# Optimization experiments

Hardware: AMD Instinct MI355X
Metric: run time of the kernel (lower is better)

Reference implementation:

```python
import jax, jax.numpy as jnp
import numpy as np

OUT_FEATURES = 11008
IN_FEATURES = 4096
PACKED_LEN = OUT_FEATURES * IN_FEATURES // 4  # 4 ternary vals per byte, 2 bits each


def setup_inputs() -> dict:
    key = jax.random.key(0)
    k1, k2, k3 = jax.random.split(key, 3)
    x = jax.random.normal(k1, (4, 1024, IN_FEATURES), dtype=jnp.float32)
    packed_weight = jax.random.randint(k2, (PACKED_LEN,), 0, 256, dtype=jnp.int32)
    weight_scale = jax.random.uniform(k3, (1,), dtype=jnp.float32)
    return {"x": x, "packed_weight": packed_weight, "weight_scale": weight_scale}


def _dequantize_weight(packed_weight, weight_scale):
    shifts = jnp.arange(0, 8, 2, dtype=jnp.int32)          # [4]
    q = ((packed_weight[:, None] >> shifts) & 3) - 1        # [P, 4]
    q = q.reshape(OUT_FEATURES, IN_FEATURES).astype(jnp.float32)
    return q * weight_scale.reshape(())                      # dequantize


def reference(x, packed_weight, weight_scale):
    w = _dequantize_weight(packed_weight, weight_scale)      # [out, in]
    # F.linear: y = x @ w.T  (bias=False)
    return jnp.einsum('bsi,oi->bso', x, w)
```

## Files before the change

kernel.cpp:

```cpp
#include <hip/hip_runtime.h>
#include <hip/hip_bf16.h>

#define OUT_F 11008
#define IN_F  4096
#define M_DIM 4096

typedef __attribute__((ext_vector_type(8))) short bf16x8;
typedef __attribute__((ext_vector_type(4))) float f32x4;
typedef __attribute__((ext_vector_type(8))) unsigned short us8;

__device__ __forceinline__ unsigned short f2bf_rne(float f) {
    unsigned u = __builtin_bit_cast(unsigned, f);
    u += 0x7fffu + ((u >> 16) & 1u);
    return (unsigned short)(u >> 16);
}

__global__ void prep_kernel(const float* __restrict__ x,
                            unsigned short* __restrict__ xb,
                            const int* __restrict__ pw,
                            unsigned char* __restrict__ pw2) {
    if (blockIdx.x < 8192) {
        size_t i = ((size_t)blockIdx.x * blockDim.x + threadIdx.x) * 8;
        float4 a = *(const float4*)(x + i);
        float4 b = *(const float4*)(x + i + 4);
        us8 o;
        o[0] = f2bf_rne(a.x); o[1] = f2bf_rne(a.y);
        o[2] = f2bf_rne(a.z); o[3] = f2bf_rne(a.w);
        o[4] = f2bf_rne(b.x); o[5] = f2bf_rne(b.y);
        o[6] = f2bf_rne(b.z); o[7] = f2bf_rne(b.w);
        *(us8*)(xb + i) = o;
    } else {
        const int kb   = blockIdx.x - 8192;
        const int kt   = kb & 63;
        const int rgrp = kb >> 6;
        const int row  = rgrp * 256 + threadIdx.x;
        const int4* src = (const int4*)(pw + (size_t)row * 1024 + kt * 16);
        unsigned out[4];
#pragma unroll
        for (int i = 0; i < 4; ++i) {
            int4 v = src[i];
            out[i] = (v.x & 0xFF) | ((v.y & 0xFF) << 8) |
                     ((v.z & 0xFF) << 16) | ((unsigned)v.w << 24);
        }
        *(uint4*)(pw2 + ((size_t)kt * OUT_F + row) * 16) =
            *(const uint4*)out;
    }
}

__device__ __forceinline__ void unpack_byte(unsigned b, unsigned& d_lo,
                                            unsigned& d_hi) {
    const unsigned PA = 0x00800080u;
    const unsigned PB = 0x403F00BFu;
    unsigned m0 = (b & 0xFu) * 0x00404101u;
    unsigned s0 = (m0 & 0x03030303u) | 0x00040004u;
    d_lo = __builtin_amdgcn_perm(PA, PB, s0);
    unsigned m1 = (b >> 4) * 0x00404101u;
    unsigned s1 = (m1 & 0x03030303u) | 0x00040004u;
    d_hi = __builtin_amdgcn_perm(PA, PB, s1);
}

__global__ __launch_bounds__(512, 2) void gemm_kernel(
    const unsigned short* __restrict__ A,
    const unsigned char* __restrict__ P,
    float* __restrict__ C,
    const float* __restrict__ scale_ptr) {
    constexpr int K  = IN_F;
    constexpr int N  = OUT_F;
    constexpr int NT = K / 64;

    __shared__ unsigned short sA[2][2][256][32];
    __shared__ unsigned short sB[2][2][256][32];
    __shared__ unsigned char  pb[2][4096];

    const int tid  = threadIdx.x;
    const int wave = tid >> 6;
    const int lane = tid & 63;
    const int quad = lane >> 4;
    const int mrow = lane & 15;
    const int sw   = quad ^ ((mrow >> 1) & 3);

    const int srow = lane >> 2;
    const int sseg = (lane & 3) ^ ((lane >> 3) & 3);

    const int lin = blockIdx.x;
    const int xcd = lin & 7;
    const int q   = lin >> 3;
    const int bm  = xcd * 2 + q / 43;
    const int bn  = q % 43;

    const int wm = (wave >> 2) * 128;
    const int wn = (wave & 3) * 64;

    const unsigned short* Ag = A + (size_t)bm * 256 * K;

    f32x4 acc[8][4];
#pragma unroll
    for (int i = 0; i < 8; i++)
#pragma unroll
        for (int j = 0; j < 4; j++) acc[i][j] = (f32x4){0.f, 0.f, 0.f, 0.f};

    auto STAGE_A = [&](int nb, int kbase) {
#pragma unroll
        for (int h = 0; h < 2; ++h) {
#pragma unroll
            for (int c = 0; c < 2; ++c) {
                const int chunk = wave * 2 + c;
                const int grow  = chunk * 16 + srow;
                const unsigned short* src =
                    Ag + (size_t)grow * K + kbase + h * 32 + sseg * 8;
                __builtin_amdgcn_global_load_lds(
                    (const __attribute__((address_space(1))) void*)src,
                    (__attribute__((address_space(3))) void*)
                        (&sA[nb][h][0][0] + chunk * 512),
                    16, 0, 0);
            }
        }
    };
    auto STAGE_P = [&](int nb, int kt) {
        if (wave < 4) {
            const unsigned char* src =
                P + ((size_t)kt * N + bn * 256 + wave * 64 + lane) * 16;
            __builtin_amdgcn_global_load_lds(
                (const __attribute__((address_space(1))) void*)src,
                (__attribute__((address_space(3))) void*)(&pb[nb][wave * 1024]),
                16, 0, 0);
        }
    };
    auto UNPACK = [&](int srcb, int dstb) {
        const int row = tid >> 1;
        const int h   = tid & 1;
        unsigned long long pk =
            *(const unsigned long long*)&pb[srcb][tid * 8];
        const int rsw = (row >> 1) & 3;
#pragma unroll
        for (int s = 0; s < 4; ++s) {
            unsigned p16 = (unsigned)(pk >> (16 * s)) & 0xFFFFu;
            unsigned d0, d1, d2, d3;
            unpack_byte(p16 & 0xFFu, d0, d1);
            unpack_byte(p16 >> 8, d2, d3);
            const int slot = s ^ rsw;
            *(uint4*)&sB[dstb][h][row][slot * 8] = (uint4){d0, d1, d2, d3};
        }
    };

    STAGE_A(0, 0);
    STAGE_P(1, 0);
    __syncthreads();
    UNPACK(1, 0);
    STAGE_P(0, 1);
    __syncthreads();

    for (int kt = 0; kt < NT; ++kt) {
        const int  buf  = kt & 1;
        const int  nbuf = buf ^ 1;
        const bool pf1  = (kt + 1 < NT);
        const bool pf2  = (kt + 2 < NT);

        if (pf1) STAGE_A(nbuf, (kt + 1) * 64);
        if (pf2) STAGE_P(nbuf, kt + 2);

        if (pf1) UNPACK(buf, nbuf);

#pragma unroll
        for (int h = 0; h < 2; ++h) {
            bf16x8 a[8], b[4];
#pragma unroll
            for (int t = 0; t < 8; ++t)
                a[t] = *(const bf16x8*)&sA[buf][h][wm + t * 16 + mrow][sw * 8];
#pragma unroll
            for (int j = 0; j < 4; ++j)
                b[j] = *(const bf16x8*)&sB[buf][h][wn + j * 16 + mrow][sw * 8];
#pragma unroll
            for (int t = 0; t < 8; ++t)
#pragma unroll
                for (int j = 0; j < 4; ++j)
                    acc[t][j] = __builtin_amdgcn_mfma_f32_16x16x32_bf16(
                        a[t], b[j], acc[t][j], 0, 0, 0);
        }

        __syncthreads();
    }

    const float scale = *scale_ptr;
    float* Cg = C + (size_t)(bm * 256 + wm) * N + bn * 256 + wn;
#pragma unroll
    for (int i = 0; i < 8; ++i) {
#pragma unroll
        for (int j = 0; j < 4; ++j) {
#pragma unroll
            for (int r = 0; r < 4; ++r) {
                const int row = i * 16 + quad * 4 + r;
                const int col = j * 16 + mrow;
                Cg[(size_t)row * N + col] = acc[i][j][r] * scale;
            }
        }
    }
}

extern "C" void kernel_launch(void* const* d_in, const int* in_sizes, int n_in,
                              void* d_out, int out_size, void* d_ws, size_t ws_size,
                              hipStream_t stream) {
    const float* x   = (const float*)d_in[0];
    const int* pw    = (const int*)d_in[1];
    const float* wsc = (const float*)d_in[2];

    float* out = (float*)d_out;

    unsigned short* xb  = (unsigned short*)d_ws;
    unsigned char*  pw2 = (unsigned char*)((char*)d_ws
                          + (size_t)M_DIM * IN_F * 2);

    prep_kernel<<<8192 + 2752, 256, 0, stream>>>(x, xb, pw, pw2);

    gemm_kernel<<<688, 512, 0, stream>>>(xb, pw2, out, wsc);
}
```

Measured before the change: 620.1 us.

## Pre-swizzle packed weights into MFMA fragment layout and unpack directly into registers

The prep kernel now transposes the packed ternary weights through shared memory into a per-lane MFMA fragment order, so each lane holds a 16-bit pack per (j,h). The GEMM no longer stages packed bytes into LDS, unpacks them into an sB tile, and reads them back. Each wave instead loads its own packed shorts from global memory into registers one tile ahead and unpacks them straight into B fragments. This removes the sB/pb LDS traffic and frees LDS. In exchange each wave of a block repeats unpack work that was shared before, and the global loads are scattered 2-byte accesses.

Result: faster. 558.2 us (-10.0%).

```diff
diff --git a/kernel.cpp b/kernel.cpp
--- a/kernel.cpp
+++ b/kernel.cpp
@@ -18,7 +18,7 @@
 __global__ void prep_kernel(const float* __restrict__ x,
                             unsigned short* __restrict__ xb,
                             const int* __restrict__ pw,
-                            unsigned char* __restrict__ pw2) {
+                            unsigned short* __restrict__ pw2) {
     if (blockIdx.x < 8192) {
         size_t i = ((size_t)blockIdx.x * blockDim.x + threadIdx.x) * 8;
         float4 a = *(const float4*)(x + i);
@@ -30,20 +30,31 @@
         o[6] = f2bf_rne(b.z); o[7] = f2bf_rne(b.w);
         *(us8*)(xb + i) = o;
     } else {
-        const int kb   = blockIdx.x - 8192;
-        const int kt   = kb & 63;
-        const int rgrp = kb >> 6;
-        const int row  = rgrp * 256 + threadIdx.x;
-        const int4* src = (const int4*)(pw + (size_t)row * 1024 + kt * 16);
-        unsigned out[4];
-#pragma unroll
-        for (int i = 0; i < 4; ++i) {
-            int4 v = src[i];
-            out[i] = (v.x & 0xFF) | ((v.y & 0xFF) << 8) |
-                     ((v.z & 0xFF) << 16) | ((unsigned)v.w << 24);
-        }
-        *(uint4*)(pw2 + ((size_t)kt * OUT_F + row) * 16) =
-            *(const uint4*)out;
+        __shared__ unsigned char lb[16 * 1028];
+        const int rg = blockIdx.x - 8192;
+        const int t  = threadIdx.x;
+        const int4* src = (const int4*)(pw + (size_t)rg * 16384);
+#pragma unroll
+        for (int r = 0; r < 16; ++r) {
+            int4 v = src[r * 256 + t];
+            lb[r * 1028 + t * 4 + 0] = (unsigned char)(v.x & 0xFF);
+            lb[r * 1028 + t * 4 + 1] = (unsigned char)(v.y & 0xFF);
+            lb[r * 1028 + t * 4 + 2] = (unsigned char)(v.z & 0xFF);
+            lb[r * 1028 + t * 4 + 3] = (unsigned char)(v.w & 0xFF);
+        }
+        __syncthreads();
+        unsigned short* dst = pw2 + (size_t)rg * 8192;
+#pragma unroll
+        for (int i = 0; i < 32; ++i) {
+            const int u    = i * 256 + t;
+            const int kt   = u >> 7;
+            const int h    = (u >> 6) & 1;
+            const int qd   = (u >> 4) & 3;
+            const int mrow = u & 15;
+            const int c0   = kt * 16 + h * 8 + qd * 2;
+            dst[u] = (unsigned short)(lb[mrow * 1028 + c0] |
+                                      (lb[mrow * 1028 + c0 + 1] << 8));
+        }
     }
 }
 
@@ -59,9 +70,17 @@
     d_hi = __builtin_amdgcn_perm(PA, PB, s1);
 }
 
+__device__ __forceinline__ bf16x8 unpack_us(unsigned short p) {
+    unsigned d0, d1, d2, d3;
+    unpack_byte(p & 0xFFu, d0, d1);
+    unpack_byte((unsigned)p >> 8, d2, d3);
+    uint4 u = (uint4){d0, d1, d2, d3};
+    return __builtin_bit_cast(bf16x8, u);
+}
+
 __global__ __launch_bounds__(512, 2) void gemm_kernel(
     const unsigned short* __restrict__ A,
-    const unsigned char* __restrict__ P,
+    const unsigned short* __restrict__ P,
     float* __restrict__ C,
     const float* __restrict__ scale_ptr) {
     constexpr int K  = IN_F;
@@ -69,8 +88,6 @@
     constexpr int NT = K / 64;
 
     __shared__ unsigned short sA[2][2][256][32];
-    __shared__ unsigned short sB[2][2][256][32];
-    __shared__ unsigned char  pb[2][4096];
 
     const int tid  = threadIdx.x;
     const int wave = tid >> 6;
@@ -92,6 +109,7 @@
     const int wn = (wave & 3) * 64;
 
     const unsigned short* Ag = A + (size_t)bm * 256 * K;
+    const int rgb = bn * 16 + (wn >> 4);
 
     f32x4 acc[8][4];
 #pragma unroll
@@ -116,60 +134,43 @@
             }
         }
     };
-    auto STAGE_P = [&](int nb, int kt) {
-        if (wave < 4) {
-            const unsigned char* src =
-                P + ((size_t)kt * N + bn * 256 + wave * 64 + lane) * 16;
-            __builtin_amdgcn_global_load_lds(
-                (const __attribute__((address_space(1))) void*)src,
-                (__attribute__((address_space(3))) void*)(&pb[nb][wave * 1024]),
-                16, 0, 0);
-        }
+
+    auto pidx = [&](int kt, int j, int h) -> size_t {
+        return (((size_t)(rgb + j) * 64 + kt) * 2 + h) * 64 + lane;
     };
-    auto UNPACK = [&](int srcb, int dstb) {
-        const int row = tid >> 1;
-        const int h   = tid & 1;
-        unsigned long long pk =
-            *(const unsigned long long*)&pb[srcb][tid * 8];
-        const int rsw = (row >> 1) & 3;
-#pragma unroll
-        for (int s = 0; s < 4; ++s) {
-            unsigned p16 = (unsigned)(pk >> (16 * s)) & 0xFFFFu;
-            unsigned d0, d1, d2, d3;
-            unpack_byte(p16 & 0xFFu, d0, d1);
-            unpack_byte(p16 >> 8, d2, d3);
-            const int slot = s ^ rsw;
-            *(uint4*)&sB[dstb][h][row][slot * 8] = (uint4){d0, d1, d2, d3};
-        }
-    };
 
     STAGE_A(0, 0);
-    STAGE_P(1, 0);
-    __syncthreads();
-    UNPACK(1, 0);
-    STAGE_P(0, 1);
+    unsigned short pkb[8], npkb[8];
+#pragma unroll
+    for (int j = 0; j < 4; ++j)
+#pragma unroll
+        for (int h = 0; h < 2; ++h) pkb[j * 2 + h] = P[pidx(0, j, h)];
+#pragma unroll
+    for (int i = 0; i < 8; ++i) npkb[i] = 0;
     __syncthreads();
 
     for (int kt = 0; kt < NT; ++kt) {
         const int  buf  = kt & 1;
         const int  nbuf = buf ^ 1;
         const bool pf1  = (kt + 1 < NT);
-        const bool pf2  = (kt + 2 < NT);
-
-        if (pf1) STAGE_A(nbuf, (kt + 1) * 64);
-        if (pf2) STAGE_P(nbuf, kt + 2);
-
-        if (pf1) UNPACK(buf, nbuf);
+
+        if (pf1) {
+            STAGE_A(nbuf, (kt + 1) * 64);
+#pragma unroll
+            for (int j = 0; j < 4; ++j)
+#pragma unroll
+                for (int h = 0; h < 2; ++h)
+                    npkb[j * 2 + h] = P[pidx(kt + 1, j, h)];
+        }
 
 #pragma unroll
         for (int h = 0; h < 2; ++h) {
             bf16x8 a[8], b[4];
 #pragma unroll
+            for (int j = 0; j < 4; ++j) b[j] = unpack_us(pkb[j * 2 + h]);
+#pragma unroll
             for (int t = 0; t < 8; ++t)
                 a[t] = *(const bf16x8*)&sA[buf][h][wm + t * 16 + mrow][sw * 8];
-#pragma unroll
-            for (int j = 0; j < 4; ++j)
-                b[j] = *(const bf16x8*)&sB[buf][h][wn + j * 16 + mrow][sw * 8];
 #pragma unroll
             for (int t = 0; t < 8; ++t)
 #pragma unroll
@@ -177,6 +178,9 @@
                     acc[t][j] = __builtin_amdgcn_mfma_f32_16x16x32_bf16(
                         a[t], b[j], acc[t][j], 0, 0, 0);
         }
+
+#pragma unroll
+        for (int i = 0; i < 8; ++i) pkb[i] = npkb[i];
 
         __syncthreads();
     }
@@ -207,10 +211,10 @@
     float* out = (float*)d_out;
 
     unsigned short* xb  = (unsigned short*)d_ws;
-    unsigned char*  pw2 = (unsigned char*)((char*)d_ws
+    unsigned short* pw2 = (unsigned short*)((char*)d_ws
                           + (size_t)M_DIM * IN_F * 2);
 
-    prep_kernel<<<8192 + 2752, 256, 0, stream>>>(x, xb, pw, pw2);
+    prep_kernel<<<8192 + 688, 256, 0, stream>>>(x, xb, pw, pw2);
 
     gemm_kernel<<<688, 512, 0, stream>>>(xb, pw2, out, wsc);
 }
```
